# Performance work log

Measured on AMD Instinct MI355X. Metric: run time of the kernel, lower is better.

## Reference

```python
import jax, jax.numpy as jnp
import numpy as np
import math

B = 16
IMG = 224
P = 16
C_IN = 3
E = 768
H = 12
HD = E // H          # 64
D = 6                # depth
MLP = 3072
NC = 1000
GH = IMG // P        # 14
N = GH * GH + 1      # 197 tokens incl cls
LAMBDA_INIT = 0.8
EPS = 1e-5


def setup_inputs() -> dict:
    key = jax.random.key(0)
    ks = jax.random.split(key, 24)
    s = 0.02
    inp = {
        "x": jax.random.normal(ks[0], (B, C_IN, IMG, IMG), jnp.float32),
        "conv_w": jax.random.normal(ks[1], (E, C_IN, P, P), jnp.float32) * s,
        "conv_b": jnp.zeros((E,), jnp.float32),
        "cls_token": jax.random.normal(ks[2], (1, 1, E), jnp.float32) * s,
        "pos_embed": jax.random.normal(ks[3], (1, N, E), jnp.float32) * s,
        # per-layer stacked params (leading dim D)
        "Wq": jax.random.normal(ks[4], (D, E, 2 * E), jnp.float32) * s,
        "Wk": jax.random.normal(ks[5], (D, E, 2 * E), jnp.float32) * s,
        "Wv": jax.random.normal(ks[6], (D, E, 2 * E), jnp.float32) * s,
        "lq1": jax.random.normal(ks[7], (D, H, HD), jnp.float32) * 0.1,
        "lk1": jax.random.normal(ks[8], (D, H, HD), jnp.float32) * 0.1,
        "lq2": jax.random.normal(ks[9], (D, H, HD), jnp.float32) * 0.1,
        "lk2": jax.random.normal(ks[10], (D, H, HD), jnp.float32) * 0.1,
        "gn_g": jnp.ones((D, 2 * HD), jnp.float32),
        "gn_b": jnp.zeros((D, 2 * HD), jnp.float32),
        "Wo": jax.random.normal(ks[11], (D, 2 * E, E), jnp.float32) * s,
        "ln1_g": jnp.ones((D, E), jnp.float32),
        "ln1_b": jnp.zeros((D, E), jnp.float32),
        "ln2_g": jnp.ones((D, E), jnp.float32),
        "ln2_b": jnp.zeros((D, E), jnp.float32),
        "mlp_w1": jax.random.normal(ks[12], (D, E, MLP), jnp.float32) * s,
        "mlp_b1": jnp.zeros((D, MLP), jnp.float32),
        "mlp_w2": jax.random.normal(ks[13], (D, MLP, E), jnp.float32) * s,
        "mlp_b2": jnp.zeros((D, E), jnp.float32),
        "lnf_g": jnp.ones((E,), jnp.float32),
        "lnf_b": jnp.zeros((E,), jnp.float32),
        "head_w": jax.random.normal(ks[14], (E, NC), jnp.float32) * s,
        "head_b": jnp.zeros((NC,), jnp.float32),
    }
    return inp


def _ln(z, g, b):
    m = jnp.mean(z, axis=-1, keepdims=True)
    v = jnp.var(z, axis=-1, keepdims=True)
    return (z - m) * jax.lax.rsqrt(v + EPS) * g + b


def _forward(x, conv_w, conv_b, cls_token, pos_embed, Wq, Wk, Wv,
             lq1, lk1, lq2, lk2, gn_g, gn_b, Wo,
             ln1_g, ln1_b, ln2_g, ln2_b,
             mlp_w1, mlp_b1, mlp_w2, mlp_b2,
             lnf_g, lnf_b, head_w, head_b):
    Bx = x.shape[0]
    # patch embedding (conv stride=kernel == non-overlapping patch matmul)
    xp = x.reshape(Bx, C_IN, GH, P, GH, P)
    tok = jnp.einsum('bchpwq,ecpq->bhwe', xp, conv_w).reshape(Bx, GH * GH, E) + conv_b
    h = jnp.concatenate([jnp.broadcast_to(cls_token, (Bx, 1, E)), tok], axis=1) + pos_embed

    scale = 1.0 / math.sqrt(HD)

    def block(h, p):
        xn = _ln(h, p['ln1_g'], p['ln1_b'])
        q = (xn @ p['Wq']).reshape(Bx, N, H, 2 * HD).transpose(0, 2, 1, 3)
        k = (xn @ p['Wk']).reshape(Bx, N, H, 2 * HD).transpose(0, 2, 1, 3)
        v = (xn @ p['Wv']).reshape(Bx, N, H, 2 * HD).transpose(0, 2, 1, 3)
        q1, q2 = q[..., :HD], q[..., HD:]
        k1, k2 = k[..., :HD], k[..., HD:]
        a1 = jax.nn.softmax(jnp.einsum('bhnd,bhmd->bhnm', q1, k1) * scale, axis=-1)
        a2 = jax.nn.softmax(jnp.einsum('bhnd,bhmd->bhnm', q2, k2) * scale, axis=-1)
        lam = (jnp.exp(jnp.sum(p['lq1'] * p['lk1'], axis=-1))
               - jnp.exp(jnp.sum(p['lq2'] * p['lk2'], axis=-1)) + LAMBDA_INIT)  # (H,)
        attn = a1 - lam[None, :, None, None] * a2
        o = jnp.einsum('bhnm,bhmd->bhnd', attn, v)  # (B,H,N,2HD)
        # GroupNorm(1 group) over (N, 2HD) per (b,h) sample, per-channel affine
        m = jnp.mean(o, axis=(2, 3), keepdims=True)
        var = jnp.var(o, axis=(2, 3), keepdims=True)
        o = (o - m) * jax.lax.rsqrt(var + EPS) * p['gn_g'] + p['gn_b']
        o = o.transpose(0, 2, 1, 3).reshape(Bx, N, 2 * E) @ p['Wo']
        h = h + o
        xn2 = _ln(h, p['ln2_g'], p['ln2_b'])
        ff = jax.nn.gelu(xn2 @ p['mlp_w1'] + p['mlp_b1'], approximate=False) @ p['mlp_w2'] + p['mlp_b2']
        return h + ff, attn

    params = dict(Wq=Wq, Wk=Wk, Wv=Wv, lq1=lq1, lk1=lk1, lq2=lq2, lk2=lk2,
                  gn_g=gn_g, gn_b=gn_b, Wo=Wo, ln1_g=ln1_g, ln1_b=ln1_b,
                  ln2_g=ln2_g, ln2_b=ln2_b, mlp_w1=mlp_w1, mlp_b1=mlp_b1,
                  mlp_w2=mlp_w2, mlp_b2=mlp_b2)
    h, attns = jax.lax.scan(block, h, params)
    h = _ln(h, lnf_g, lnf_b)
    logits = h[:, 0] @ head_w + head_b
    return logits, attns  # attns: (D, B, H, N, N)


def reference(x, conv_w, conv_b, cls_token, pos_embed, Wq, Wk, Wv,
              lq1, lk1, lq2, lk2, gn_g, gn_b, Wo,
              ln1_g, ln1_b, ln2_g, ln2_b,
              mlp_w1, mlp_b1, mlp_w2, mlp_b2,
              lnf_g, lnf_b, head_w, head_b):
    return _forward(x, conv_w, conv_b, cls_token, pos_embed, Wq, Wk, Wv,
                    lq1, lk1, lq2, lk2, gn_g, gn_b, Wo,
                    ln1_g, ln1_b, ln2_g, ln2_b,
                    mlp_w1, mlp_b1, mlp_w2, mlp_b2,
                    lnf_g, lnf_b, head_w, head_b)
```

## Files before the change

kernel.cpp:

```cpp
#include <hip/hip_runtime.h>
#include <hip/hip_bf16.h>
#include <math.h>

#define BB 16
#define NT 197
#define EE 768
#define HH 12
#define E2 1536
#define MLPD 3072
#define NCLS 1000
#define ND 6
#define EPSF 1e-5f
#define SCALEF 0.125f
#define LAMINIT 0.8f
#define TOKC 3152

using v8bf  = __attribute__((ext_vector_type(8))) __bf16;
using f32x4 = __attribute__((ext_vector_type(4))) float;
typedef __hip_bfloat16 bf16;

#define AS1 __attribute__((address_space(1)))
#define AS3 __attribute__((address_space(3)))

__device__ __forceinline__ void gld16(const void* g, void* l) {
    __builtin_amdgcn_global_load_lds((const AS1 void*)g, (AS3 void*)l, 16, 0, 0);
}

__device__ __forceinline__ float gelu_f(float x) {
    const float u = x + 0.044715f * x * x * x;
    const float e = __expf(fminf(1.5957691216f * u, 80.f));
    return x * e / (e + 1.f);
}

__global__ __launch_bounds__(256) void gemm_bf16(
    const bf16* __restrict__ A, const bf16* __restrict__ Wt,
    const float* __restrict__ bias, float* __restrict__ C0,
    float* __restrict__ C1, float* __restrict__ C2,
    const float* __restrict__ pos, int M, int K, int ldA, int ldB, int Nc, int mode)
{
    __shared__ __align__(16) unsigned char smem[32768];
    const int t = threadIdx.x;
    const int wave = t >> 6, lane = t & 63;
    const int wr = wave >> 1, wc = wave & 1;
    const int lr = lane & 15, lk = lane >> 4;

    const int bid0 = blockIdx.y * gridDim.x + blockIdx.x;
    const int nwg = gridDim.x * gridDim.y;
    const int qv = nwg >> 3, rv = nwg & 7;
    const int xcd = bid0 & 7, ii = bid0 >> 3;
    const int wgid = (xcd < rv ? xcd * (qv + 1) : rv * (qv + 1) + (xcd - rv) * qv) + ii;
    const int rowBase = (wgid / gridDim.x) * 128;
    const int colBase = (wgid % gridDim.x) * 128;
    const size_t zoff = (size_t)blockIdx.z * K * 2;

    f32x4 acc[4][4];
#pragma unroll
    for (int i = 0; i < 4; ++i)
#pragma unroll
        for (int j = 0; j < 4; ++j) acc[i][j] = (f32x4){0.f,0.f,0.f,0.f};

    const size_t ldA2 = (size_t)ldA * 2, ldB2 = (size_t)ldB * 2;
    const int srow = t >> 3;
    const int schunk = (t & 7) ^ ((t >> 3) & 7);
    const char* Abase = (const char*)A + zoff + schunk * 16;
    const char* Bbase = (const char*)Wt + zoff + schunk * 16;
    unsigned char* lA = smem + t * 16;
    unsigned char* lB = smem + 16384 + t * 16;
    const v8bf* Sa = (const v8bf*)smem;
    const v8bf* Sb = (const v8bf*)(smem + 16384);

    int rA[4], rB[4];
#pragma unroll
    for (int c = 0; c < 4; ++c) {
        rA[c] = min(rowBase + c * 32 + srow, M - 1);
        rB[c] = colBase + c * 32 + srow;
    }

    for (int k0 = 0; k0 < K; k0 += 64) {
        const size_t kb = (size_t)k0 * 2;
#pragma unroll
        for (int c = 0; c < 4; ++c) {
            gld16(Abase + (size_t)rA[c] * ldA2 + kb, lA + c * 4096);
            gld16(Bbase + (size_t)rB[c] * ldB2 + kb, lB + c * 4096);
        }
        __syncthreads();
#pragma unroll
        for (int s = 0; s < 2; ++s) {
            const int xr_ = (s * 4 + lk) ^ (lr & 7);
            v8bf af[4], bfr[4];
#pragma unroll
            for (int i = 0; i < 4; ++i) af[i] = Sa[(wr * 64 + i * 16 + lr) * 8 + xr_];
#pragma unroll
            for (int j = 0; j < 4; ++j) bfr[j] = Sb[(wc * 64 + j * 16 + lr) * 8 + xr_];
#pragma unroll
            for (int i = 0; i < 4; ++i)
#pragma unroll
                for (int j = 0; j < 4; ++j)
                    acc[i][j] = __builtin_amdgcn_mfma_f32_16x16x32_bf16(af[i], bfr[j], acc[i][j], 0, 0, 0);
        }
        __syncthreads();
    }

    if (mode == 0) {
        float* Cs = (float*)smem;
        float* C0z = C0 + (size_t)blockIdx.z * M * Nc;
#pragma unroll
        for (int half = 0; half < 2; ++half) {
            __syncthreads();
            if (wr == half) {
#pragma unroll
                for (int i = 0; i < 4; ++i)
#pragma unroll
                    for (int j = 0; j < 4; ++j)
#pragma unroll
                        for (int rr = 0; rr < 4; ++rr)
                            Cs[(i*16 + lk*4 + rr)*128 + wc*64 + j*16 + lr] = acc[i][j][rr];
            }
            __syncthreads();
#pragma unroll
            for (int k = 0; k < 8; ++k) {
                const int idx = k*256 + t;
                const int row = idx >> 5, c4 = idx & 31;
                const int r = rowBase + half*64 + row;
                if (r < M)
                    *(float4*)&C0z[(size_t)r*Nc + colBase + c4*4] = *(float4*)&Cs[row*128 + c4*4];
            }
        }
    } else if (mode == 1) {
        const int which = colBase / E2;
        if (which == 2) {
#pragma unroll
            for (int i = 0; i < 4; ++i)
#pragma unroll
                for (int j = 0; j < 4; ++j)
#pragma unroll
                    for (int rr = 0; rr < 4; ++rr) {
                        const int r = rowBase + wr * 64 + i * 16 + lk * 4 + rr;
                        const int c = colBase + wc * 64 + j * 16 + lr;
                        if (r >= M) continue;
                        const int b_ = r / NT, n_ = r % NT;
                        const int cc = c % E2;
                        const int h_ = cc >> 7, d_ = cc & 127;
                        const size_t bh = (size_t)(b_ * HH + h_);
                        ((bf16*)C2)[((bh * 7 + (n_ >> 5)) * 8 + (d_ >> 4)) * 512 +
                                    (size_t)(((d_ & 15) + (((n_ >> 3) & 3) << 4)) * 8 + (n_ & 7))] =
                            __float2bfloat16(acc[i][j][rr]);
                    }
        } else {
            const int hFix = (colBase % E2) >> 7;
            bf16* dstBase = (bf16*)(which == 0 ? C0 : C1);
            bf16* Cs = (bf16*)smem;
            __syncthreads();
#pragma unroll
            for (int i = 0; i < 4; ++i)
#pragma unroll
                for (int j = 0; j < 4; ++j)
#pragma unroll
                    for (int rr = 0; rr < 4; ++rr)
                        Cs[(wr*64 + i*16 + lk*4 + rr)*128 + wc*64 + j*16 + lr] =
                            __float2bfloat16(acc[i][j][rr]);
            __syncthreads();
#pragma unroll
            for (int k = 0; k < 8; ++k) {
                const int idx = k*256 + t;
                const int row = idx >> 4, c8 = idx & 15;
                const int r = rowBase + row;
                if (r < M) {
                    const int b_ = r / NT, n_ = r - b_ * NT;
                    const size_t bh = (size_t)(b_ * HH + hFix);
                    *(uint4*)(dstBase + (bh * 208 + n_) * 128 + c8 * 8) =
                        *(uint4*)&Cs[row*128 + c8*8];
                }
            }
        }
    } else if (mode == 3) {
        bf16* Cs = (bf16*)smem;
        __syncthreads();
#pragma unroll
        for (int i = 0; i < 4; ++i)
#pragma unroll
            for (int j = 0; j < 4; ++j)
#pragma unroll
                for (int rr = 0; rr < 4; ++rr) {
                    const int c = colBase + wc*64 + j*16 + lr;
                    float val = acc[i][j][rr] + bias[c];
                    Cs[(wr*64 + i*16 + lk*4 + rr)*128 + wc*64 + j*16 + lr] =
                        __float2bfloat16(gelu_f(val));
                }
        __syncthreads();
        bf16* C0b = (bf16*)C0;
#pragma unroll
        for (int k = 0; k < 8; ++k) {
            const int idx = k*256 + t;
            const int row = idx >> 4, c8 = idx & 15;
            const int r = rowBase + row;
            if (r < M)
                *(uint4*)(C0b + (size_t)r*Nc + colBase + c8*8) = *(uint4*)&Cs[row*128 + c8*8];
        }
    } else {
#pragma unroll
        for (int i = 0; i < 4; ++i)
#pragma unroll
            for (int j = 0; j < 4; ++j)
#pragma unroll
                for (int rr = 0; rr < 4; ++rr) {
                    const int r = rowBase + wr * 64 + i * 16 + lk * 4 + rr;
                    const int c = colBase + wc * 64 + j * 16 + lr;
                    if (r >= M) continue;
                    const int b_ = r / 196, p_ = r % 196;
                    C0[((size_t)(b_ * NT) + 1 + p_) * EE + c] =
                        acc[i][j][rr] + bias[c] + pos[(size_t)(1 + p_) * EE + c];
                }
    }
}

template<int NF>
__global__ __launch_bounds__(512, 2) void gemm256t(
    const bf16* __restrict__ A, const bf16* __restrict__ Wt,
    const float* __restrict__ bias, float* __restrict__ C0,
    float* __restrict__ C1, float* __restrict__ C2,
    int M, int K, int Nc, int mode)
{
    constexpr int NB = NF * 64;
    constexpr int BUFSZ = 32768 + NF * 8192;
    __shared__ __align__(16) unsigned char smem[2 * BUFSZ];
    const int t = threadIdx.x;
    const int wave = t >> 6, lane = t & 63;
    const int wm = wave >> 2, wn = wave & 3;
    const int lr = lane & 15, lk = lane >> 4;

    const int bid0 = blockIdx.y * gridDim.x + blockIdx.x;
    const int nwg = gridDim.x * gridDim.y;
    const int qv = nwg >> 3, rv = nwg & 7;
    const int xcd = bid0 & 7, ii = bid0 >> 3;
    const int wgid = (xcd < rv ? xcd * (qv + 1) : rv * (qv + 1) + (xcd - rv) * qv) + ii;
    const int rowBase = (wgid / gridDim.x) * 256;
    const int colBase = (wgid % gridDim.x) * NB;

    f32x4 acc[8][NF];
#pragma unroll
    for (int i = 0; i < 8; ++i)
#pragma unroll
        for (int j = 0; j < NF; ++j) acc[i][j] = (f32x4){0.f,0.f,0.f,0.f};

    const size_t ldK2 = (size_t)K * 2;
    const int srow = t >> 3;
    const int schunk = (t & 7) ^ (srow & 7);
    const char* Abase = (const char*)A + schunk * 16;
    const char* Bbase = (const char*)Wt + schunk * 16;

    int rA[4], rB[NF];
#pragma unroll
    for (int p = 0; p < 4; ++p) rA[p] = min(rowBase + p * 64 + srow, M - 1);
#pragma unroll
    for (int p = 0; p < NF; ++p) rB[p] = colBase + p * 64 + srow;

    {
        unsigned char* l0 = smem + t * 16;
#pragma unroll
        for (int p = 0; p < 4; ++p) gld16(Abase + (size_t)rA[p] * ldK2, l0 + p * 8192);
#pragma unroll
        for (int p = 0; p < NF; ++p) gld16(Bbase + (size_t)rB[p] * ldK2, l0 + 32768 + p * 8192);
#pragma unroll
        for (int p = 0; p < 4; ++p) gld16(Abase + (size_t)rA[p] * ldK2 + 128, l0 + BUFSZ + p * 8192);
#pragma unroll
        for (int p = 0; p < NF; ++p) gld16(Bbase + (size_t)rB[p] * ldK2 + 128, l0 + BUFSZ + 32768 + p * 8192);
        if constexpr (NF == 4) asm volatile("s_waitcnt vmcnt(8)" ::: "memory");
        else                   asm volatile("s_waitcnt vmcnt(7)" ::: "memory");
        asm volatile("s_barrier" ::: "memory");
    }

    const int NTt = K >> 6;
    for (int kt = 0; kt < NTt; ++kt) {
        const int buf = kt & 1;
        const v8bf* Sa = (const v8bf*)(smem + buf * BUFSZ);
        const v8bf* Sb = (const v8bf*)(smem + buf * BUFSZ + 32768);

        v8bf bfr[2][NF], af[2][4];
#pragma unroll
        for (int s = 0; s < 2; ++s) {
            const int x0 = s * 4 + lk;
#pragma unroll
            for (int j = 0; j < NF; ++j) {
                const int row = wn * (NF * 16) + j * 16 + lr;
                bfr[s][j] = Sb[row * 8 + (x0 ^ (lr & 7))];
            }
#pragma unroll
            for (int i = 0; i < 4; ++i) {
                const int row = wm * 128 + i * 16 + lr;
                af[s][i] = Sa[row * 8 + (x0 ^ (lr & 7))];
            }
        }
        __builtin_amdgcn_s_setprio(1);
#pragma unroll
        for (int s = 0; s < 2; ++s)
#pragma unroll
            for (int i = 0; i < 4; ++i)
#pragma unroll
                for (int j = 0; j < NF; ++j)
                    acc[i][j] = __builtin_amdgcn_mfma_f32_16x16x32_bf16(af[s][i], bfr[s][j], acc[i][j], 0, 0, 0);
        __builtin_amdgcn_s_setprio(0);

        v8bf af2[2][4];
#pragma unroll
        for (int s = 0; s < 2; ++s)
#pragma unroll
            for (int i = 0; i < 4; ++i) {
                const int row = wm * 128 + 64 + i * 16 + lr;
                af2[s][i] = Sa[row * 8 + ((s * 4 + lk) ^ (lr & 7))];
            }
        asm volatile("s_waitcnt lgkmcnt(0)" ::: "memory");
        asm volatile("s_barrier" ::: "memory");
        if (kt + 2 < NTt) {
            const size_t kb = (size_t)(kt + 2) * 128;
            unsigned char* ld = smem + buf * BUFSZ + t * 16;
#pragma unroll
            for (int p = 0; p < 4; ++p) gld16(Abase + (size_t)rA[p] * ldK2 + kb, ld + p * 8192);
#pragma unroll
            for (int p = 0; p < NF; ++p) gld16(Bbase + (size_t)rB[p] * ldK2 + kb, ld + 32768 + p * 8192);
            if constexpr (NF == 4) asm volatile("s_waitcnt vmcnt(8)" ::: "memory");
            else                   asm volatile("s_waitcnt vmcnt(7)" ::: "memory");
        } else {
            asm volatile("s_waitcnt vmcnt(0)" ::: "memory");
        }
        asm volatile("s_barrier" ::: "memory");
        __builtin_amdgcn_s_setprio(1);
#pragma unroll
        for (int s = 0; s < 2; ++s)
#pragma unroll
            for (int i = 0; i < 4; ++i)
#pragma unroll
                for (int j = 0; j < NF; ++j)
                    acc[4 + i][j] = __builtin_amdgcn_mfma_f32_16x16x32_bf16(af2[s][i], bfr[s][j], acc[4 + i][j], 0, 0, 0);
        __builtin_amdgcn_s_setprio(0);
    }

    if constexpr (NF == 4) {
        if (mode == 1) {
            const int which = colBase / E2;
            if (which == 2) {
#pragma unroll
                for (int i = 0; i < 8; ++i)
#pragma unroll
                    for (int j = 0; j < 4; ++j)
#pragma unroll
                        for (int rr = 0; rr < 4; ++rr) {
                            const int r = rowBase + wm * 128 + i * 16 + lk * 4 + rr;
                            if (r >= M) continue;
                            const int c = colBase + wn * 64 + j * 16 + lr;
                            const int b_ = r / NT, n_ = r % NT;
                            const int cc = c % E2;
                            const int h_ = cc >> 7, d_ = cc & 127;
                            const size_t bh = (size_t)(b_ * HH + h_);
                            ((bf16*)C2)[((bh * 7 + (n_ >> 5)) * 8 + (d_ >> 4)) * 512 +
                                        (size_t)(((d_ & 15) + (((n_ >> 3) & 3) << 4)) * 8 + (n_ & 7))] =
                                __float2bfloat16(acc[i][j][rr]);
                        }
            } else {
                bf16* dstBase = (bf16*)(which == 0 ? C0 : C1);
                const int h0 = (colBase % E2) >> 7;
                bf16* Cs = (bf16*)smem;
                __syncthreads();
#pragma unroll
                for (int i = 0; i < 8; ++i)
#pragma unroll
                    for (int j = 0; j < 4; ++j)
#pragma unroll
                        for (int rr = 0; rr < 4; ++rr)
                            Cs[(wm*128 + i*16 + lk*4 + rr)*256 + wn*64 + j*16 + lr] =
                                __float2bfloat16(acc[i][j][rr]);
                __syncthreads();
#pragma unroll
                for (int k = 0; k < 16; ++k) {
                    const int idx = k * 512 + t;
                    const int row = idx >> 5, c8 = idx & 31;
                    const int r = rowBase + row;
                    if (r < M) {
                        const int b_ = r / NT, n_ = r - b_ * NT;
                        const size_t bh = (size_t)(b_ * HH + h0 + (c8 >> 4));
                        *(uint4*)(dstBase + (bh * 208 + n_) * 128 + (size_t)(c8 & 15) * 8) =
                            *(uint4*)&Cs[row * 256 + c8 * 8];
                    }
                }
            }
            return;
        }
    }
    {
        bf16* Cs = (bf16*)smem;
        __syncthreads();
#pragma unroll
        for (int i = 0; i < 8; ++i)
#pragma unroll
            for (int j = 0; j < NF; ++j) {
                const int c = colBase + wn * (NF * 16) + j * 16 + lr;
                const float bv = bias[c];
#pragma unroll
                for (int rr = 0; rr < 4; ++rr)
                    Cs[(wm*128 + i*16 + lk*4 + rr)*NB + wn*(NF*16) + j*16 + lr] =
                        __float2bfloat16(gelu_f(acc[i][j][rr] + bv));
            }
        __syncthreads();
        bf16* C0b = (bf16*)C0;
        constexpr int CW = NB / 8;
        constexpr int ITER = 256 * CW / 512;
#pragma unroll
        for (int k = 0; k < ITER; ++k) {
            const int idx = k * 512 + t;
            const int row = idx / CW, c8 = idx - row * CW;
            const int r = rowBase + row;
            if (r < M)
                *(uint4*)(C0b + (size_t)r * Nc + colBase + c8 * 8) =
                    *(uint4*)&Cs[row * NB + c8 * 8];
        }
    }
}

__global__ __launch_bounds__(64) void attn_mfma(
    const bf16* __restrict__ Qrm, const bf16* __restrict__ Krm,
    const bf16* __restrict__ Vf, const float* __restrict__ lamp,
    float* __restrict__ aout, float* __restrict__ o, float* __restrict__ stats)
{
    const int lane = threadIdx.x;
    const int fid = blockIdx.x;
    const int xcd = fid & 7, rest = fid >> 3;
    const int qt = rest % 13, g = rest / 13;
    const int bh = g * 8 + xcd;
    const int hh = bh % HH;
    const int lr = lane & 15, lk = lane >> 4;

    __shared__ __align__(16) bf16 P[16][232];

    {
        const int r = lane & 15, c0 = 192 + (lane >> 4) * 10;
#pragma unroll
        for (int j = 0; j < 10; ++j) P[r][c0 + j] = __float2bfloat16(0.f);
    }

    v8bf qa[4];
    const bf16* Qb = Qrm + ((size_t)bh * 208 + qt * 16) * 128;
#pragma unroll
    for (int kk = 0; kk < 4; ++kk)
        qa[kk] = *(const v8bf*)(Qb + lr * 128 + kk * 32 + lk * 8);

    const bf16* Kb = Krm + (size_t)bh * 208 * 128;
    const f32x4 zf = {0.f, 0.f, 0.f, 0.f};
    f32x4 s1[13], s2[13];
#pragma unroll
    for (int t = 0; t < 13; ++t) {
        const bf16* Kt = Kb + (t * 16 + lr) * 128 + lk * 8;
        const v8bf k0 = *(const v8bf*)(Kt);
        const v8bf k1 = *(const v8bf*)(Kt + 32);
        const v8bf k2 = *(const v8bf*)(Kt + 64);
        const v8bf k3 = *(const v8bf*)(Kt + 96);
        s1[t] = __builtin_amdgcn_mfma_f32_16x16x32_bf16(qa[1], k1,
                __builtin_amdgcn_mfma_f32_16x16x32_bf16(qa[0], k0, zf, 0, 0, 0), 0, 0, 0);
        s2[t] = __builtin_amdgcn_mfma_f32_16x16x32_bf16(qa[3], k3,
                __builtin_amdgcn_mfma_f32_16x16x32_bf16(qa[2], k2, zf, 0, 0, 0), 0, 0, 0);
    }

    float m1[4] = {-1e30f,-1e30f,-1e30f,-1e30f}, m2[4] = {-1e30f,-1e30f,-1e30f,-1e30f};
#pragma unroll
    for (int t = 0; t < 13; ++t) {
        const bool kv = (t * 16 + lr) < NT;
#pragma unroll
        for (int rr = 0; rr < 4; ++rr) {
            s1[t][rr] = kv ? s1[t][rr] * SCALEF : -1e30f;
            s2[t][rr] = kv ? s2[t][rr] * SCALEF : -1e30f;
            m1[rr] = fmaxf(m1[rr], s1[t][rr]);
            m2[rr] = fmaxf(m2[rr], s2[t][rr]);
        }
    }
#pragma unroll
    for (int off = 8; off >= 1; off >>= 1)
#pragma unroll
        for (int rr = 0; rr < 4; ++rr) {
            m1[rr] = fmaxf(m1[rr], __shfl_xor(m1[rr], off));
            m2[rr] = fmaxf(m2[rr], __shfl_xor(m2[rr], off));
        }

    float z1[4] = {0,0,0,0}, z2[4] = {0,0,0,0};
#pragma unroll
    for (int t = 0; t < 13; ++t)
#pragma unroll
        for (int rr = 0; rr < 4; ++rr) {
            const float e1 = __expf(s1[t][rr] - m1[rr]);
            const float e2 = __expf(s2[t][rr] - m2[rr]);
            s1[t][rr] = e1; s2[t][rr] = e2;
            z1[rr] += e1; z2[rr] += e2;
        }
#pragma unroll
    for (int off = 8; off >= 1; off >>= 1)
#pragma unroll
        for (int rr = 0; rr < 4; ++rr) {
            z1[rr] += __shfl_xor(z1[rr], off);
            z2[rr] += __shfl_xor(z2[rr], off);
        }
    const float lam = lamp[hh];
    float r1[4], r2[4];
#pragma unroll
    for (int rr = 0; rr < 4; ++rr) { r1[rr] = 1.f / z1[rr]; r2[rr] = lam / z2[rr]; }

    __syncthreads();
#pragma unroll
    for (int t = 0; t < 13; ++t) {
        const int m_ = t * 16 + lr;
#pragma unroll
        for (int rr = 0; rr < 4; ++rr) {
            const float p = s1[t][rr] * r1[rr] - s2[t][rr] * r2[rr];
            const int n_ = lk * 4 + rr;
            P[n_][m_] = __float2bfloat16(p);
            const int n_g = qt * 16 + n_;
            if (m_ < NT && n_g < NT)
                aout[((size_t)bh * NT + n_g) * NT + m_] = p;
        }
    }
    __syncthreads();

    f32x4 oacc[8];
#pragma unroll
    for (int dt = 0; dt < 8; ++dt) oacc[dt] = zf;
    const v8bf* Vp = (const v8bf*)(Vf + (size_t)bh * 7 * 8 * 512);
    const bf16* Pb = &P[0][0];
#pragma unroll
    for (int mk = 0; mk < 7; ++mk) {
        const v8bf pa = *(const v8bf*)(Pb + lr * 232 + mk * 32 + lk * 8);
#pragma unroll
        for (int dt = 0; dt < 8; ++dt)
            oacc[dt] = __builtin_amdgcn_mfma_f32_16x16x32_bf16(
                pa, Vp[(mk * 8 + dt) * 64 + lane], oacc[dt], 0, 0, 0);
    }
#pragma unroll
    for (int dt = 0; dt < 8; ++dt)
#pragma unroll
        for (int rr = 0; rr < 4; ++rr) {
            const int n_g = qt * 16 + lk * 4 + rr;
            if (n_g < NT)
                o[((size_t)bh * NT + n_g) * 128 + dt * 16 + lr] = oacc[dt][rr];
        }

    float s = 0.f, ss = 0.f;
#pragma unroll
    for (int dt = 0; dt < 8; ++dt)
#pragma unroll
        for (int rr = 0; rr < 4; ++rr) {
            const int n_g = qt * 16 + lk * 4 + rr;
            const float vv = (n_g < NT) ? oacc[dt][rr] : 0.f;
            s += vv; ss += vv * vv;
        }
#pragma unroll
    for (int off = 32; off >= 1; off >>= 1) {
        s  += __shfl_xor(s, off);
        ss += __shfl_xor(ss, off);
    }
    if (lane == 0) {
        stats[(bh * 13 + qt) * 2]     = s;
        stats[(bh * 13 + qt) * 2 + 1] = ss;
    }
}

__global__ __launch_bounds__(256) void gn_apply(
    const float* __restrict__ o, const float* __restrict__ stats,
    const float* __restrict__ g, const float* __restrict__ bb, bf16* __restrict__ o2)
{
    const int bh = blockIdx.y, qq = blockIdx.x;
    const int t = threadIdx.x;
    float S = 0.f, SS = 0.f;
#pragma unroll
    for (int j = 0; j < 13; ++j) {
        S  += stats[(bh * 13 + j) * 2];
        SS += stats[(bh * 13 + j) * 2 + 1];
    }
    const float inv = 1.f / (float)(NT * 128);
    const float mean = S * inv;
    const float var  = SS * inv - mean * mean;
    const float rstd = rsqrtf(var + EPSF);
    const int b_ = bh / HH, h_ = bh % HH;
    const float4* ob = (const float4*)(o + (size_t)bh * NT * 128);
    const float4* g4 = (const float4*)g;
    const float4* b4 = (const float4*)bb;
    for (int idx = t; idx < 50 * 32; idx += 256) {
        const int n_ = qq * 50 + (idx >> 5);
        if (n_ >= NT) continue;
        const int d4 = idx & 31;
        const float4 v4 = ob[n_ * 32 + d4];
        const float4 gg = g4[d4], bv = b4[d4];
        bf16 tmp[4];
        tmp[0] = __float2bfloat16((v4.x - mean) * rstd * gg.x + bv.x);
        tmp[1] = __float2bfloat16((v4.y - mean) * rstd * gg.y + bv.y);
        tmp[2] = __float2bfloat16((v4.z - mean) * rstd * gg.z + bv.z);
        tmp[3] = __float2bfloat16((v4.w - mean) * rstd * gg.w + bv.w);
        *(uint2*)(o2 + ((size_t)(b_ * NT + n_)) * E2 + h_ * 128 + d4 * 4) = *(uint2*)tmp;
    }
}

__global__ __launch_bounds__(256) void ln_rows(
    const float* __restrict__ in, const float* __restrict__ g,
    const float* __restrict__ bb, bf16* __restrict__ out)
{
    const int r = blockIdx.x;
    const int t = threadIdx.x;
    const float* x = in + (size_t)r * EE;
    const float v0 = x[t], v1 = x[t+256], v2 = x[t+512];
    __shared__ float rs[256], rss[256];
    rs[t]  = v0+v1+v2;
    rss[t] = v0*v0+v1*v1+v2*v2;
    __syncthreads();
    for (int st = 128; st > 0; st >>= 1) {
        if (t < st) { rs[t] += rs[t+st]; rss[t] += rss[t+st]; }
        __syncthreads();
    }
    const float mean = rs[0] * (1.f/768.f);
    const float var  = rss[0] * (1.f/768.f) - mean*mean;
    const float rstd = rsqrtf(var + EPSF);
    bf16* o = out + (size_t)r * EE;
    o[t]     = __float2bfloat16((v0-mean)*rstd*g[t]     + bb[t]);
    o[t+256] = __float2bfloat16((v1-mean)*rstd*g[t+256] + bb[t+256]);
    o[t+512] = __float2bfloat16((v2-mean)*rstd*g[t+512] + bb[t+512]);
}

__global__ __launch_bounds__(192) void ln_fuse(
    const float* __restrict__ hin, const float* __restrict__ Pp,
    const float* __restrict__ bias, const float* __restrict__ g,
    const float* __restrict__ bb, float* __restrict__ hout, bf16* __restrict__ xout)
{
    const int r = blockIdx.x;
    const int t = threadIdx.x;
    const int lane = t & 63, wv = t >> 6;
    const size_t base4 = (size_t)r * 192 + t;
    float4 v = ((const float4*)hin)[base4];
    const float4 p0 = ((const float4*)Pp)[base4];
    const float4 p1 = ((const float4*)Pp)[(size_t)TOKC * 192 + base4];
    v.x += p0.x + p1.x; v.y += p0.y + p1.y; v.z += p0.z + p1.z; v.w += p0.w + p1.w;
    if (bias) {
        const float4 bv = ((const float4*)bias)[t];
        v.x += bv.x; v.y += bv.y; v.z += bv.z; v.w += bv.w;
    }
    float s  = v.x + v.y + v.z + v.w;
    float ss = v.x*v.x + v.y*v.y + v.z*v.z + v.w*v.w;
#pragma unroll
    for (int off = 32; off >= 1; off >>= 1) {
        s  += __shfl_xor(s, off);
        ss += __shfl_xor(ss, off);
    }
    __shared__ float ws_[3][2];
    if (lane == 0) { ws_[wv][0] = s; ws_[wv][1] = ss; }
    __syncthreads();
    const float S  = ws_[0][0] + ws_[1][0] + ws_[2][0];
    const float SS = ws_[0][1] + ws_[1][1] + ws_[2][1];
    const float mean = S * (1.f/768.f);
    const float var  = SS * (1.f/768.f) - mean*mean;
    const float rstd = rsqrtf(var + EPSF);
    ((float4*)hout)[base4] = v;
    const float4 gg = ((const float4*)g)[t];
    const float4 bv2 = ((const float4*)bb)[t];
    bf16 tmp[4];
    tmp[0] = __float2bfloat16((v.x-mean)*rstd*gg.x + bv2.x);
    tmp[1] = __float2bfloat16((v.y-mean)*rstd*gg.y + bv2.y);
    tmp[2] = __float2bfloat16((v.z-mean)*rstd*gg.z + bv2.z);
    tmp[3] = __float2bfloat16((v.w-mean)*rstd*gg.w + bv2.w);
    *(uint2*)(xout + base4 * 4) = *(uint2*)tmp;
}

__global__ void setup_misc(const float* __restrict__ conv_w, bf16* __restrict__ cwbf,
                           const float* __restrict__ cls, const float* __restrict__ pos,
                           float* __restrict__ h,
                           const float* __restrict__ lq1, const float* __restrict__ lk1,
                           const float* __restrict__ lq2, const float* __restrict__ lk2,
                           float* __restrict__ lam)
{
    const int bid = blockIdx.x;
    if (bid < 2304) {
        const int i = bid * 256 + threadIdx.x;
        cwbf[i] = __float2bfloat16(conv_w[i]);
    } else if (bid < 2352) {
        const int i = (bid - 2304) * 256 + threadIdx.x;
        const int b_ = i / EE, e_ = i % EE;
        h[(size_t)(b_*NT)*EE + e_] = cls[e_] + pos[e_];
    } else {
        const int i = threadIdx.x;
        if (i < ND*HH) {
            float d1 = 0.f, d2 = 0.f;
            for (int d = 0; d < 64; ++d) {
                d1 += lq1[i*64+d]*lk1[i*64+d];
                d2 += lq2[i*64+d]*lk2[i*64+d];
            }
            lam[i] = expf(d1) - expf(d2) + LAMINIT;
        }
    }
}

__global__ void im2col_kernel(const float* __restrict__ x, bf16* __restrict__ xcol)
{
    const int i = blockIdx.x*256 + threadIdx.x;
    if (i >= 3136*EE) return;
    const int kidx = i % EE;
    const int p_ = i / EE;
    const int b_ = p_ / 196;
    const int pp = p_ % 196;
    const int gh = pp / 14, gw = pp % 14;
    const int c_ = kidx >> 8, rr = (kidx >> 4) & 15, q_ = kidx & 15;
    xcol[i] = __float2bfloat16(x[((size_t)(b_*3 + c_)*224 + gh*16 + rr)*224 + gw*16 + q_]);
}

__global__ __launch_bounds__(256) void transpose_pack(
    const float* __restrict__ Wq, const float* __restrict__ Wk,
    const float* __restrict__ Wv, const float* __restrict__ Wo,
    const float* __restrict__ W1, const float* __restrict__ W2,
    bf16* __restrict__ wall)
{
    __shared__ __align__(16) float tile[64 * 256];
    int bid = blockIdx.x;
    const int dl = bid / 576; bid -= dl * 576;
    bf16* wq_t = wall + (size_t)dl * 9437184;
    bf16* wo_t = wq_t + 3538944;
    bf16* w1_t = wo_t + 1179648;
    bf16* w2_t = w1_t + 2359296;
    const float* src; bf16* dst; int K, N, gx;
    if (bid < 216) {
        const int z = bid / 72; bid -= z * 72;
        src = (z == 0 ? Wq : (z == 1 ? Wk : Wv)) + (size_t)dl * EE * E2;
        dst = wq_t + (size_t)z * E2 * EE; K = EE; N = E2; gx = 6;
    } else if (bid < 288) { src = Wo + (size_t)dl*E2*EE;   dst = wo_t; K = E2;   N = EE;   gx = 3;  bid -= 216; }
    else if (bid < 432)   { src = W1 + (size_t)dl*EE*MLPD; dst = w1_t; K = EE;   N = MLPD; gx = 12; bid -= 288; }
    else                  { src = W2 + (size_t)dl*MLPD*EE; dst = w2_t; K = MLPD; N = EE;   gx = 3;  bid -= 432; }
    const int bx = bid % gx, by = bid / gx;
    const int n0 = bx * 256, k0 = by * 64;
    const int t = threadIdx.x;
    const int lane = t & 63, wv = t >> 6;

    {
        char* ldsb = (char*)tile + lane * 16;
#pragma unroll
        for (int j = 0; j < 16; ++j) {
            const int r = wv * 16 + j;
            const float* sp = src + (size_t)(k0 + r) * N + n0 + ((lane ^ r) << 2);
            gld16(sp, ldsb + r * 1024);
        }
    }
    asm volatile("s_waitcnt vmcnt(0)" ::: "memory");
    __syncthreads();

    const int c16 = t >> 2, sub = t & 3;
    float v[64];
#pragma unroll
    for (int k = 0; k < 64; ++k)
        v[k] = tile[k * 256 + (((c16 ^ k) & 63) << 2) + sub];
    bf16 a[64];
#pragma unroll
    for (int k = 0; k < 64; ++k) a[k] = __float2bfloat16(v[k]);
    bf16* d = dst + (size_t)(n0 + t) * K + k0;
#pragma unroll
    for (int q = 0; q < 8; ++q)
        *(uint4*)(d + q * 8) = *(uint4*)&a[q * 8];
}

__global__ __launch_bounds__(256) void ln_cls(
    const float* __restrict__ h, const float* __restrict__ g,
    const float* __restrict__ bb, float* __restrict__ xr)
{
    const int b_ = blockIdx.x;
    const int t = threadIdx.x;
    const float* x = h + (size_t)(b_*NT)*EE;
    const float v0 = x[t], v1 = x[t+256], v2 = x[t+512];
    __shared__ float rs[256], rss[256];
    rs[t]  = v0+v1+v2;
    rss[t] = v0*v0+v1*v1+v2*v2;
    __syncthreads();
    for (int st = 128; st > 0; st >>= 1) {
        if (t < st) { rs[t] += rs[t+st]; rss[t] += rss[t+st]; }
        __syncthreads();
    }
    const float mean = rs[0] * (1.f/768.f);
    const float var  = rss[0] * (1.f/768.f) - mean*mean;
    const float rstd = rsqrtf(var + EPSF);
    float* o = xr + (size_t)b_ * EE;
    o[t]     = (v0-mean)*rstd*g[t]     + bb[t];
    o[t+256] = (v1-mean)*rstd*g[t+256] + bb[t+256];
    o[t+512] = (v2-mean)*rstd*g[t+512] + bb[t+512];
}

__global__ __launch_bounds__(256) void head_gemm(
    const float* __restrict__ xr, const float* __restrict__ hw,
    const float* __restrict__ hb, float* __restrict__ logits)
{
    const int b_ = blockIdx.y, ct = blockIdx.x;
    const int t = threadIdx.x;
    const int c_loc = t & 63, kp = t >> 6;
    const int c = ct * 64 + c_loc;
    __shared__ float xs[768];
    for (int i = t; i < 768; i += 256) xs[i] = xr[(size_t)b_*EE + i];
    __syncthreads();
    float acc = 0.f;
    if (c < NCLS) {
        const int k0 = kp * 192;
        for (int kk = k0; kk < k0 + 192; ++kk)
            acc += xs[kk] * hw[(size_t)kk * NCLS + c];
    }
    __shared__ float red[4][64];
    red[kp][c_loc] = acc;
    __syncthreads();
    if (kp == 0 && c < NCLS)
        logits[(size_t)b_*NCLS + c] =
            red[0][c_loc] + red[1][c_loc] + red[2][c_loc] + red[3][c_loc] + hb[c];
}

extern "C" void kernel_launch(void* const* d_in, const int* in_sizes, int n_in,
                              void* d_out, int out_size, void* d_ws, size_t ws_size,
                              hipStream_t stream)
{
    const float* x      = (const float*)d_in[0];
    const float* conv_w = (const float*)d_in[1];
    const float* conv_b = (const float*)d_in[2];
    const float* cls    = (const float*)d_in[3];
    const float* pos    = (const float*)d_in[4];
    const float* Wq     = (const float*)d_in[5];
    const float* Wk     = (const float*)d_in[6];
    const float* Wv     = (const float*)d_in[7];
    const float* lq1    = (const float*)d_in[8];
    const float* lk1    = (const float*)d_in[9];
    const float* lq2    = (const float*)d_in[10];
    const float* lk2    = (const float*)d_in[11];
    const float* gn_g   = (const float*)d_in[12];
    const float* gn_b   = (const float*)d_in[13];
    const float* Wo     = (const float*)d_in[14];
    const float* ln1_g  = (const float*)d_in[15];
    const float* ln1_b  = (const float*)d_in[16];
    const float* ln2_g  = (const float*)d_in[17];
    const float* ln2_b  = (const float*)d_in[18];
    const float* mlp_w1 = (const float*)d_in[19];
    const float* mlp_b1 = (const float*)d_in[20];
    const float* mlp_w2 = (const float*)d_in[21];
    const float* mlp_b2 = (const float*)d_in[22];
    const float* lnf_g  = (const float*)d_in[23];
    const float* lnf_b  = (const float*)d_in[24];
    const float* head_w = (const float*)d_in[25];
    const float* head_b = (const float*)d_in[26];

    float* out_f    = (float*)d_out;
    float* logits   = out_f;
    float* attn_out = out_f + (size_t)BB*NCLS;

    const int TOK = TOKC;
    const size_t TOKE = (size_t)TOK*EE;

    float* ws   = (float*)d_ws;
    float* h    = ws;
    float* o    = h + TOKE;
    float* Pp   = o + (size_t)BB*HH*NT*128;
    bf16*  Qrm  = (bf16*)(Pp + 2*TOKE);
    bf16*  Krm  = Qrm + (size_t)192*208*128;
    bf16*  Vf   = Krm + (size_t)192*208*128;
    bf16*  act2 = Vf + (size_t)192*7*8*512;
    bf16*  xn   = act2 + (size_t)TOK*MLPD;
    bf16*  wall = xn + TOKE;
    bf16*  cwbf = wall + (size_t)6*9437184;
    float* lam  = (float*)(cwbf + (size_t)EE*EE);
    float* xr   = lam + 128;
    float* gnst = xr + (size_t)BB*EE;

    hipMemsetAsync(Vf, 0, (size_t)192*7*8*512*2, stream);

    setup_misc<<<2353, 256, 0, stream>>>(conv_w, cwbf, cls, pos, h,
                                         lq1, lk1, lq2, lk2, lam);
    transpose_pack<<<6*576, 256, 0, stream>>>(Wq, Wk, Wv, Wo, mlp_w1, mlp_w2, wall);
    im2col_kernel<<<(3136*EE+255)/256, 256, 0, stream>>>(x, xn);
    gemm_bf16<<<dim3(EE/128, 25), 256, 0, stream>>>(
        xn, cwbf, conv_b, h, nullptr, nullptr, pos, 3136, EE, EE, EE, EE, 4);

    ln_rows<<<TOK, 256, 0, stream>>>(h, ln1_g, ln1_b, xn);

    for (int dl = 0; dl < ND; ++dl) {
        bf16* wq_t = wall + (size_t)dl*9437184;
        bf16* wo_t = wq_t + 3538944;
        bf16* w1_t = wo_t + 1179648;
        bf16* w2_t = w1_t + 2359296;

        gemm256t<4><<<dim3(4608/256, (TOK+255)/256), 512, 0, stream>>>(
            xn, wq_t, nullptr, (float*)Qrm, (float*)Krm, (float*)Vf,
            TOK, EE, 4608, 1);
        attn_mfma<<<2496, 64, 0, stream>>>(
            Qrm, Krm, Vf, lam + dl*HH, attn_out + (size_t)dl*BB*HH*NT*NT, o, gnst);
        gn_apply<<<dim3(4, BB*HH), 256, 0, stream>>>(
            o, gnst, gn_g + dl*128, gn_b + dl*128, act2);
        gemm_bf16<<<dim3(EE/128, 25, 2), 256, 0, stream>>>(
            act2, wo_t, nullptr, Pp, nullptr, nullptr, nullptr,
            TOK, E2/2, E2, E2, EE, 0);
        ln_fuse<<<TOK, 192, 0, stream>>>(
            h, Pp, nullptr, ln2_g + dl*EE, ln2_b + dl*EE, h, xn);
        gemm256t<3><<<dim3(MLPD/192, (TOK+255)/256), 512, 0, stream>>>(
            xn, w1_t, mlp_b1 + dl*MLPD, (float*)act2, nullptr, nullptr,
            TOK, EE, MLPD, 3);
        gemm_bf16<<<dim3(EE/128, 25, 2), 256, 0, stream>>>(
            act2, w2_t, nullptr, Pp, nullptr, nullptr, nullptr,
            TOK, MLPD/2, MLPD, MLPD, EE, 0);
        if (dl < ND-1)
            ln_fuse<<<TOK, 192, 0, stream>>>(
                h, Pp, mlp_b2 + dl*EE, ln1_g + (dl+1)*EE, ln1_b + (dl+1)*EE, h, xn);
        else
            ln_fuse<<<TOK, 192, 0, stream>>>(
                h, Pp, mlp_b2 + dl*EE, lnf_g, lnf_b, h, xn);
    }

    ln_cls<<<BB, 256, 0, stream>>>(h, lnf_g, lnf_b, xr);
    head_gemm<<<dim3(16, BB), 256, 0, stream>>>(xr, head_w, head_b, logits);
}
```

Baseline: 1.387 ms.

## Restructure weight transpose-pack to stage bf16 tiles in LDS for coalesced writes

Reworks the fp32-to-bf16 weight transpose kernel. Each block now covers a 384x64 output tile, loading three 128x64 fp32 sub-tiles and converting them into a swizzled bf16 LDS buffer. The result is then written out as full 768-byte contiguous rows instead of each thread writing 128-byte scattered row pieces. This aims to improve global write coalescing and reduce block count. In exchange it adds more LDS use and extra barriers per block, and the reads go through an unswizzled fp32 staging tile that may hit bank conflicts.

```diff
diff --git a/kernel.cpp b/kernel.cpp
--- a/kernel.cpp
+++ b/kernel.cpp
@@ -709,50 +709,74 @@
     const float* __restrict__ W1, const float* __restrict__ W2,
     bf16* __restrict__ wall)
 {
-    __shared__ __align__(16) float tile[64 * 256];
+    __shared__ __align__(16) float tin[128 * 64];
+    __shared__ __align__(16) bf16  tout[64 * 384];
     int bid = blockIdx.x;
-    const int dl = bid / 576; bid -= dl * 576;
+    const int dl = bid / 384; bid -= dl * 384;
     bf16* wq_t = wall + (size_t)dl * 9437184;
     bf16* wo_t = wq_t + 3538944;
     bf16* w1_t = wo_t + 1179648;
     bf16* w2_t = w1_t + 2359296;
-    const float* src; bf16* dst; int K, N, gx;
-    if (bid < 216) {
-        const int z = bid / 72; bid -= z * 72;
+    const float* src; bf16* dst; int srcN, dstK, n0, k0;
+    if (bid < 144) {
+        const int z = bid / 48; const int r = bid - z * 48;
         src = (z == 0 ? Wq : (z == 1 ? Wk : Wv)) + (size_t)dl * EE * E2;
-        dst = wq_t + (size_t)z * E2 * EE; K = EE; N = E2; gx = 6;
-    } else if (bid < 288) { src = Wo + (size_t)dl*E2*EE;   dst = wo_t; K = E2;   N = EE;   gx = 3;  bid -= 216; }
-    else if (bid < 432)   { src = W1 + (size_t)dl*EE*MLPD; dst = w1_t; K = EE;   N = MLPD; gx = 12; bid -= 288; }
-    else                  { src = W2 + (size_t)dl*MLPD*EE; dst = w2_t; K = MLPD; N = EE;   gx = 3;  bid -= 432; }
-    const int bx = bid % gx, by = bid / gx;
-    const int n0 = bx * 256, k0 = by * 64;
+        dst = wq_t + (size_t)z * E2 * EE;
+        srcN = E2; dstK = EE;
+        n0 = (r >> 1) * 64; k0 = (r & 1) * 384;
+    } else if (bid < 192) {
+        const int r = bid - 144;
+        src = Wo + (size_t)dl * E2 * EE; dst = wo_t;
+        srcN = EE; dstK = E2;
+        n0 = (r >> 2) * 64; k0 = (r & 3) * 384;
+    } else if (bid < 288) {
+        const int r = bid - 192;
+        src = W1 + (size_t)dl * EE * MLPD; dst = w1_t;
+        srcN = MLPD; dstK = EE;
+        n0 = (r >> 1) * 64; k0 = (r & 1) * 384;
+    } else {
+        const int r = bid - 288;
+        src = W2 + (size_t)dl * MLPD * EE; dst = w2_t;
+        srcN = EE; dstK = MLPD;
+        n0 = (r >> 3) * 64; k0 = (r & 7) * 384;
+    }
     const int t = threadIdx.x;
-    const int lane = t & 63, wv = t >> 6;
-
-    {
-        char* ldsb = (char*)tile + lane * 16;
-#pragma unroll
-        for (int j = 0; j < 16; ++j) {
-            const int r = wv * 16 + j;
-            const float* sp = src + (size_t)(k0 + r) * N + n0 + ((lane ^ r) << 2);
-            gld16(sp, ldsb + r * 1024);
-        }
-    }
-    asm volatile("s_waitcnt vmcnt(0)" ::: "memory");
-    __syncthreads();
-
-    const int c16 = t >> 2, sub = t & 3;
-    float v[64];
-#pragma unroll
-    for (int k = 0; k < 64; ++k)
-        v[k] = tile[k * 256 + (((c16 ^ k) & 63) << 2) + sub];
-    bf16 a[64];
-#pragma unroll
-    for (int k = 0; k < 64; ++k) a[k] = __float2bfloat16(v[k]);
-    bf16* d = dst + (size_t)(n0 + t) * K + k0;
-#pragma unroll
-    for (int q = 0; q < 8; ++q)
-        *(uint4*)(d + q * 8) = *(uint4*)&a[q * 8];
+    const int c = t & 63, kq = t >> 6;
+
+    for (int sub = 0; sub < 3; ++sub) {
+        {
+            const int row16 = t >> 4, nc = (t & 15) * 4;
+            char* ldsb = (char*)tin;
+#pragma unroll
+            for (int i = 0; i < 8; ++i) {
+                const int kr = i * 16 + row16;
+                gld16(src + (size_t)(k0 + sub * 128 + kr) * srcN + n0 + nc,
+                      ldsb + kr * 256 + (t & 15) * 16);
+            }
+        }
+        asm volatile("s_waitcnt vmcnt(0)" ::: "memory");
+        __syncthreads();
+        bf16 a[32];
+#pragma unroll
+        for (int j = 0; j < 32; ++j)
+            a[j] = __float2bfloat16(tin[(kq * 32 + j) * 64 + c]);
+#pragma unroll
+        for (int m = 0; m < 4; ++m) {
+            const int kchunk = sub * 16 + kq * 4 + m;
+            const int phys = (kchunk & ~7) | ((kchunk ^ c) & 7);
+            *(uint4*)((char*)tout + c * 768 + phys * 16) = *(uint4*)&a[m * 8];
+        }
+        __syncthreads();
+    }
+
+#pragma unroll
+    for (int it = 0; it < 12; ++it) {
+        const int idx = it * 256 + t;
+        const int r = idx / 48, ch = idx - r * 48;
+        const int phys = (ch & ~7) | ((ch ^ r) & 7);
+        *(uint4*)(dst + (size_t)(n0 + r) * dstK + k0 + ch * 8) =
+            *(uint4*)((char*)tout + r * 768 + phys * 16);
+    }
 }
 
 __global__ __launch_bounds__(256) void ln_cls(
@@ -863,7 +887,7 @@
 
     setup_misc<<<2353, 256, 0, stream>>>(conv_w, cwbf, cls, pos, h,
                                          lq1, lk1, lq2, lk2, lam);
-    transpose_pack<<<6*576, 256, 0, stream>>>(Wq, Wk, Wv, Wo, mlp_w1, mlp_w2, wall);
+    transpose_pack<<<6*384, 256, 0, stream>>>(Wq, Wk, Wv, Wo, mlp_w1, mlp_w2, wall);
     im2col_kernel<<<(3136*EE+255)/256, 256, 0, stream>>>(x, xn);
     gemm_bf16<<<dim3(EE/128, 25), 256, 0, stream>>>(
         xn, cwbf, conv_b, h, nullptr, nullptr, pos, 3136, EE, EE, EE, EE, 4);
```

After: 1.381 ms, median of 2. No clear change (-0.4%).
